# Optimization experiments

Measured on AMD Instinct MI355X. Metric: run time of the kernel, lower is better.

Reference implementation:

```python
import jax, jax.numpy as jnp
import numpy as np

N, E, DIN, GB, GD, LB, LD, G = 50000, 640000, 64, 128, 4, 256, 2, 1024


def setup_inputs() -> dict:
    key = jax.random.key(0)
    ks = jax.random.split(key, 20)
    p = lambda k, shape: (jax.random.normal(k, shape, dtype=jnp.float32) * 0.05)
    return {
        "x": jax.random.normal(ks[0], (N, DIN), dtype=jnp.float32),
        "edge_index": jax.random.randint(ks[1], (2, E), 0, N, dtype=jnp.int64),
        "batch": jnp.sort(jax.random.randint(ks[2], (N,), 0, G, dtype=jnp.int64)),
        "num_graphs": G,
        "W0": p(ks[3], (DIN, GB)), "b0": p(ks[4], (GB,)),
        "Wg": p(ks[5], (GD, GB, GB)), "bg": p(ks[6], (GD, GB)),
        "gamma_g": jnp.ones((GD, GB), jnp.float32), "beta_g": jnp.zeros((GD, GB), jnp.float32),
        "Wl0": p(ks[7], (GB, LB)), "bl0": p(ks[8], (LB,)),
        "Wl": p(ks[9], (LD, LB, LB)), "bl": p(ks[10], (LD, LB)),
        "gamma_l": jnp.ones((LD, LB), jnp.float32), "beta_l": jnp.zeros((LD, LB), jnp.float32),
        "Wout": p(ks[11], (LB, 2)), "bout": p(ks[12], (2,)),
    }


def reference(x, edge_index, batch, num_graphs, W0, b0, Wg, bg, gamma_g, beta_g,
              Wl0, bl0, Wl, bl, gamma_l, beta_l, Wout, bout):
    n = x.shape[0]
    src, dst = edge_index[0], edge_index[1]
    # GCN degree normalization with self loops: deg = 1 + in-degree
    deg = jax.ops.segment_sum(jnp.ones(src.shape[0], x.dtype), dst, num_segments=n) + 1.0
    dinv = jax.lax.rsqrt(deg)                 # deg^{-1/2}
    enorm = dinv[src] * dinv[dst]             # [E] edge norm
    snorm = dinv * dinv                       # [N] self-loop norm (deg^{-1})

    def gcn(h, W, b):
        hw = h @ W                                            # [N, GB]
        agg = jax.ops.segment_sum(hw[src] * enorm[:, None], dst, num_segments=n)
        return agg + hw * snorm[:, None] + b

    def bn(h, g, bt):  # training-mode batchnorm (biased var), eps=1e-5
        m = h.mean(0)
        v = h.var(0)
        return (h - m) * jax.lax.rsqrt(v + 1e-5) * g + bt

    h = jax.nn.relu(gcn(x, W0, b0))
    for i in range(Wg.shape[0]):
        h = jax.nn.relu(bn(gcn(h, Wg[i], bg[i]), gamma_g[i], beta_g[i]))
    # global_add_pool
    hp = jax.ops.segment_sum(h, batch, num_segments=num_graphs)  # [G, GB]
    h = jax.nn.relu(hp @ Wl0 + bl0)
    for i in range(Wl.shape[0]):
        h = jax.nn.relu(bn(h @ Wl[i] + bl[i], gamma_l[i], beta_l[i]))
    return h @ Wout + bout
```

## Files before the change

kernel.cpp:

```cpp
#include <hip/hip_runtime.h>

#define NN 50000
#define EE 640000
#define DINv 64
#define GBv 128
#define GDv 4
#define LBv 256
#define LDv 2
#define GGv 1024

#define NB 196
#define BCAP 4096
#define BTILE 4096
#define NBT ((EE + BTILE - 1) / BTILE)

#define NTILES ((NN + 63) / 64)
#define UPN (NN * 16)
#define CONVN (DINv * GBv + GDv * GBv * GBv)

typedef _Float16 f16x8 __attribute__((ext_vector_type(8)));
typedef float f32x4 __attribute__((ext_vector_type(4)));

__device__ __forceinline__ float h2f(ushort u) {
  union { ushort u; _Float16 h; } x;
  x.u = u;
  return (float)x.h;
}
__device__ __forceinline__ ushort f2h(float f) {
  union { ushort u; _Float16 h; } x;
  x.h = (_Float16)f;
  return x.u;
}


__global__ __launch_bounds__(256) void k_bucket(const int* __restrict__ ei,
                                                int* __restrict__ bcnt,
                                                uint* __restrict__ bkt) {
  __shared__ int lcnt[NB];
  __shared__ int lbase[NB];
  __shared__ int gbase[NB];
  __shared__ int ls[256];
  __shared__ uint stage[BTILE];
  __shared__ ushort sb[BTILE];
  int tid = threadIdx.x;
  int t0 = blockIdx.x * BTILE;
  int cnt = min(BTILE, EE - t0);
  for (int i = tid; i < NB; i += 256) lcnt[i] = 0;
  __syncthreads();

  uint en[16];
  int bb[16], rk[16];
  int nper = (cnt + 255) >> 8;
  for (int k = 0; k < nper; k++) {
    int e = k * 256 + tid;
    if (e < cnt) {
      int src = ei[t0 + e];
      int dst = ei[EE + t0 + e];
      int b = dst >> 8;
      en[k] = ((uint)src << 8) | (uint)(dst & 255);
      bb[k] = b;
      rk[k] = atomicAdd(&lcnt[b], 1);
    } else {
      bb[k] = -1;
    }
  }
  __syncthreads();

  int v = (tid < NB) ? lcnt[tid] : 0;
  ls[tid] = v;
  __syncthreads();
  for (int off = 1; off < 256; off <<= 1) {
    int t = (tid >= off) ? ls[tid - off] : 0;
    __syncthreads();
    ls[tid] += t;
    __syncthreads();
  }
  if (tid < NB) {
    lbase[tid] = ls[tid] - v;
    gbase[tid] = atomicAdd(&bcnt[tid], v);
  }
  __syncthreads();

  for (int k = 0; k < nper; k++) {
    if (bb[k] >= 0) {
      int slot = lbase[bb[k]] + rk[k];
      stage[slot] = en[k];
      sb[slot] = (ushort)bb[k];
    }
  }
  __syncthreads();

  for (int i = tid; i < cnt; i += 256) {
    int b = sb[i];
    bkt[(size_t)b * BCAP + gbase[b] + (i - lbase[b])] = stage[i];
  }
}


__global__ __launch_bounds__(256) void k_csr(const uint* __restrict__ bkt,
                                             const int* __restrict__ bcnt,
                                             int* __restrict__ offs,
                                             float* __restrict__ dinv,
                                             int* __restrict__ col,
                                             int* __restrict__ deg,
                                             int* __restrict__ ghist) {
  __shared__ int lhist[256];
  __shared__ int lofs[256];
  __shared__ int lcur[256];
  __shared__ int lsb[256];
  __shared__ int lh2[64];
  int b = blockIdx.x;
  int tid = threadIdx.x;
  int bv = (tid < NB) ? bcnt[tid] : 0;
  lsb[tid] = bv;
  lhist[tid] = 0;
  if (tid < 64) lh2[tid] = 0;
  __syncthreads();
  for (int off = 1; off < 256; off <<= 1) {
    int t = (tid >= off) ? lsb[tid - off] : 0;
    __syncthreads();
    lsb[tid] += t;
    __syncthreads();
  }
  int cnt = bcnt[b];
  int base = lsb[b] - cnt;
  const uint* B = bkt + (size_t)b * BCAP;
  for (int i = tid; i < cnt; i += 256) atomicAdd(&lhist[B[i] & 255], 1);
  __syncthreads();
  int v = lhist[tid];
  lofs[tid] = v;
  __syncthreads();
  for (int off = 1; off < 256; off <<= 1) {
    int t = (tid >= off) ? lofs[tid - off] : 0;
    __syncthreads();
    lofs[tid] += t;
    __syncthreads();
  }
  int excl = lofs[tid] - v;
  int n = b * 256 + tid;
  if (n < NN) {
    offs[n] = base + excl;
    dinv[n] = rsqrtf((float)(v + 1));
    int d = min(v, 63);
    deg[n] = d;
    atomicAdd(&lh2[d], 1);
  }
  lcur[tid] = excl;
  __syncthreads();
  if (tid < 64 && lh2[tid]) atomicAdd(&ghist[tid], lh2[tid]);
  if (b == 0 && tid == 0) offs[NN] = EE;
  for (int i = tid; i < cnt; i += 256) {
    uint e = B[i];
    int p = atomicAdd(&lcur[e & 255], 1);
    col[base + p] = (int)(e >> 8);
  }
}


__global__ __launch_bounds__(256) void k_dperm(const int* __restrict__ deg,
                                               const int* __restrict__ ghist,
                                               int* __restrict__ gcur,
                                               int* __restrict__ perm) {
  __shared__ int lhist[64];
  __shared__ int lbase[64];
  int tid = threadIdx.x;
  if (tid < 64) lhist[tid] = 0;
  __syncthreads();
  int n = blockIdx.x * 256 + tid;
  int d = 0, rk = 0;
  if (n < NN) {
    d = deg[n];
    rk = atomicAdd(&lhist[d], 1);
  }
  __syncthreads();
  if (tid < 64) {
    int s = 0;
    for (int i = tid + 1; i < 64; i++) s += ghist[i];
    if (lhist[tid]) lbase[tid] = s + atomicAdd(&gcur[tid], lhist[tid]);
  }
  __syncthreads();
  if (n < NN) perm[lbase[d] + rk] = n;
}


__global__ __launch_bounds__(256) void k_prep(const float* __restrict__ x,
                                              const float* __restrict__ dinv,
                                              const float* __restrict__ W0,
                                              const float* __restrict__ Wg,
                                              ushort* __restrict__ u,
                                              ushort* __restrict__ Wt0,
                                              ushort* __restrict__ Wtg) {
  int idx = blockIdx.x * 256 + threadIdx.x;
  if (idx < UPN) {
    int n = idx >> 4;
    float4 v = ((const float4*)x)[idx];
    float d = dinv[n];
    union { ushort us[4]; uint2 q; } o;
    o.us[0] = f2h(v.x * d);
    o.us[1] = f2h(v.y * d);
    o.us[2] = f2h(v.z * d);
    o.us[3] = f2h(v.w * d);
    ((uint2*)u)[idx] = o.q;
  } else {
    int j = idx - UPN;
    if (j < DINv * GBv) {
      int c = j >> 6, k = j & 63;
      Wt0[j] = f2h(W0[k * GBv + c]);
    } else if (j < CONVN) {
      int e = j - DINv * GBv;
      int i = e >> 14, rem = e & 16383;
      int c = rem >> 7, k = rem & 127;
      Wtg[e] = f2h(Wg[i * GBv * GBv + k * GBv + c]);
    }
  }
}


template <int K, int MODE, bool STATS, bool OUTF>
__global__ __launch_bounds__(512, 4) void k_layer(const ushort* __restrict__ Gin,
                                                  const int* __restrict__ col,
                                                  const int* __restrict__ offs,
                                                  const float* __restrict__ dinv,
                                                  const int* __restrict__ perm,
                                                  const float* __restrict__ st,
                                                  const float* __restrict__ gamma,
                                                  const float* __restrict__ beta,
                                                  const ushort* __restrict__ Wt,
                                                  const float* __restrict__ bias,
                                                  float* __restrict__ stG,
                                                  ushort* __restrict__ Gout) {
  constexpr int VEC = K / 16;
  constexpr int KP = K + 8;
  constexpr int CP = 136;
  constexpr bool REUSE = (K == 128);
  __shared__ __attribute__((aligned(16))) _Float16 sW[128 * KP];
  __shared__ __attribute__((aligned(16))) _Float16 sA[64 * KP];
  __shared__ float sB[128], sS[128], sT[128];
  __shared__ float ssum[128], ssq[128];
  __shared__ float sDn[64];
  _Float16* sC = REUSE ? sA : sW;
  int tid = threadIdx.x;

  {
    constexpr int CH = K / 8;
    for (int i = tid; i < 128 * CH; i += 512) {
      int c = i / CH, ch = i - c * CH;
      *(uint4*)&sW[c * KP + ch * 8] = ((const uint4*)Wt)[i];
    }
  }
  if (tid < 128) {
    sB[tid] = bias[tid];
    if constexpr (STATS) {
      ssum[tid] = 0.f;
      ssq[tid] = 0.f;
    }
    if constexpr (MODE == 2) {
      float mu = st[tid] * (1.f / NN);
      float var = st[128 + tid] * (1.f / NN) - mu * mu;
      float s = rsqrtf(var + 1e-5f) * gamma[tid];
      sS[tid] = s;
      sT[tid] = beta[tid] - mu * s;
    }
  }
  if constexpr (MODE == 2) __syncthreads();

  int w = tid >> 6, lane = tid & 63;
  int quad = lane >> 4, m = lane & 15;
  int row0 = blockIdx.x * 64;

  float sc[VEC], tc[VEC];
  if constexpr (MODE == 2) {
#pragma unroll
    for (int v = 0; v < VEC; v++) {
      sc[v] = sS[m * VEC + v];
      tc[v] = sT[m * VEC + v];
    }
  }

  union U { uint4 v4; uint2 v2; ushort us[8]; };
  auto loadrow = [&](int s) {
    U u;
    const ushort* p = Gin + (long)s * K + m * VEC;
    if constexpr (VEC == 8) u.v4 = *(const uint4*)p;
    else u.v2 = *(const uint2*)p;
    return u;
  };

  for (int rnd = 0; rnd < 2; rnd++) {
    int r = rnd * 32 + w * 4 + quad;
    int idx = row0 + r;
    float acc[VEC];
#pragma unroll
    for (int v = 0; v < VEC; v++) acc[v] = 0.f;
    float dn = 0.f;
    if (idx < NN) {
      int n = perm[idx];
      dn = dinv[n];
      auto addrow = [&](U u, float wv) {
#pragma unroll
        for (int v = 0; v < VEC; v++) {
          float g = h2f(u.us[v]);
          if constexpr (MODE == 2) g = fmaxf(g * sc[v] + tc[v], 0.f);
          else if constexpr (MODE == 1) g = fmaxf(g, 0.f);
          acc[v] += g * wv;
        }
      };
      addrow(loadrow(n), (MODE == 0) ? 1.f : dn);
      int s0 = offs[n], s1 = offs[n + 1];
      for (int j = s0; j < s1; j += 8) {
        int si[8];
#pragma unroll
        for (int t = 0; t < 8; t++) {
          int jj = j + t;
          si[t] = col[jj < s1 ? jj : s1 - 1];
        }
        U uu[8];
#pragma unroll
        for (int t = 0; t < 8; t++) uu[t] = loadrow(si[t]);
        float wt[8];
#pragma unroll
        for (int t = 0; t < 8; t++) {
          float base = (MODE == 0) ? 1.f : dinv[si[t]];
          wt[t] = (j + t < s1) ? base : 0.f;
        }
#pragma unroll
        for (int t = 0; t < 8; t++) addrow(uu[t], wt[t]);
      }
    }
    if constexpr (OUTF) {
      if (m == 0) sDn[r] = dn;
    }
    U o;
#pragma unroll
    for (int v = 0; v < VEC; v++) o.us[v] = f2h(acc[v] * dn);
    _Float16* ap = &sA[r * KP + m * VEC];
    if constexpr (VEC == 8) *(uint4*)ap = o.v4;
    else *(uint2*)ap = o.v2;
  }
  __syncthreads();

  int wr = w >> 1, wc = w & 1;
  f32x4 acc2[4];
#pragma unroll
  for (int ct = 0; ct < 4; ct++) acc2[ct] = (f32x4){0.f, 0.f, 0.f, 0.f};
  const _Float16* pa = &sA[(16 * wr + m) * KP + quad * 8];
#pragma unroll
  for (int ks = 0; ks < K; ks += 32) {
    f16x8 a = *(const f16x8*)(pa + ks);
#pragma unroll
    for (int ct = 0; ct < 4; ct++) {
      int c = wc * 64 + ct * 16 + m;
      f16x8 bfr = *(const f16x8*)&sW[c * KP + ks + quad * 8];
      acc2[ct] = __builtin_amdgcn_mfma_f32_16x16x32_f16(a, bfr, acc2[ct], 0, 0, 0);
    }
  }

  int crow = 16 * wr + quad * 4;
  float ps[4], pq[4];
  if constexpr (STATS) {
#pragma unroll
    for (int ct = 0; ct < 4; ct++) {
      int c = wc * 64 + ct * 16 + m;
      float bb = sB[c];
      ps[ct] = 0.f;
      pq[ct] = 0.f;
#pragma unroll
      for (int r = 0; r < 4; r++) {
        if (row0 + crow + r < NN) {
          float g = acc2[ct][r] + bb;
          ps[ct] += g;
          pq[ct] += g * g;
        }
      }
    }
  }
  __syncthreads();

  float dvr[4];
  if constexpr (OUTF) {
#pragma unroll
    for (int r = 0; r < 4; r++) dvr[r] = sDn[crow + r];
  }
#pragma unroll
  for (int ct = 0; ct < 4; ct++) {
    int c = wc * 64 + ct * 16 + m;
    float bb = sB[c];
#pragma unroll
    for (int r = 0; r < 4; r++) {
      float y = acc2[ct][r] + bb;
      if constexpr (OUTF) y = fmaxf(y, 0.f) * dvr[r];
      sC[(crow + r) * CP + c] = (_Float16)y;
    }
  }
  __syncthreads();

  {
    int r = tid >> 3;
    int c0 = (tid & 7) * 16;
    int idx2 = row0 + r;
    if (idx2 < NN) {
      int node = perm[idx2];
      const uint4* srcp = (const uint4*)&sC[r * CP + c0];
      uint4* dst = (uint4*)(Gout + (long)node * 128 + c0);
      dst[0] = srcp[0];
      dst[1] = srcp[1];
    }
  }

  if constexpr (STATS) {
#pragma unroll
    for (int ct = 0; ct < 4; ct++) {
      float s = ps[ct], q = pq[ct];
      s += __shfl_xor(s, 16);
      q += __shfl_xor(q, 16);
      s += __shfl_xor(s, 32);
      q += __shfl_xor(q, 32);
      if (quad == 0) {
        atomicAdd(&ssum[wc * 64 + ct * 16 + m], s);
        atomicAdd(&ssq[wc * 64 + ct * 16 + m], q);
      }
    }
    __syncthreads();
    if (tid < 128) {
      int c = (tid + blockIdx.x * 8) & 127;
      atomicAdd(&stG[c], ssum[c]);
      atomicAdd(&stG[128 + c], ssq[c]);
    }
  }
}


__global__ __launch_bounds__(128) void k_pool2(const ushort* __restrict__ G,
                                               const float* __restrict__ st,
                                               const float* __restrict__ gamma,
                                               const float* __restrict__ beta,
                                               const int* __restrict__ batch,
                                               float* __restrict__ hp) {
  __shared__ int sse[2];
  int g = blockIdx.x;
  int c = threadIdx.x;
  if (c < 2) {
    int key = g + c;
    int lo = 0, hi = NN;
    while (lo < hi) {
      int mid = (lo + hi) >> 1;
      if (batch[mid] < key) lo = mid + 1;
      else hi = mid;
    }
    sse[c] = lo;
  }
  __syncthreads();
  int s = sse[0], e = sse[1];
  float m = st[c] * (1.f / NN);
  float v = st[128 + c] * (1.f / NN) - m * m;
  float sc = rsqrtf(v + 1e-5f) * gamma[c];
  float tc = beta[c] - m * sc;
  float a0 = 0.f, a1 = 0.f, a2 = 0.f, a3 = 0.f;
  int n = s;
  for (; n + 3 < e; n += 4) {
    float g0 = h2f(G[(long)(n + 0) * 128 + c]);
    float g1 = h2f(G[(long)(n + 1) * 128 + c]);
    float g2 = h2f(G[(long)(n + 2) * 128 + c]);
    float g3 = h2f(G[(long)(n + 3) * 128 + c]);
    a0 += fmaxf(g0 * sc + tc, 0.f);
    a1 += fmaxf(g1 * sc + tc, 0.f);
    a2 += fmaxf(g2 * sc + tc, 0.f);
    a3 += fmaxf(g3 * sc + tc, 0.f);
  }
  for (; n < e; n++) a0 += fmaxf(h2f(G[(long)n * 128 + c]) * sc + tc, 0.f);
  hp[(long)g * 128 + c] = (a0 + a1) + (a2 + a3);
}


__global__ void k_colstats(const float* __restrict__ X, int rows, float* __restrict__ st) {
  int c = threadIdx.x;
  int C = blockDim.x;
  float s = 0.f, q = 0.f;
  for (int r = blockIdx.x; r < rows; r += gridDim.x) {
    float v = X[(long)r * C + c];
    s += v;
    q += v * v;
  }
  atomicAdd(&st[c], s);
  atomicAdd(&st[C + c], q);
}


template <int KIN, int MODE>
__global__ __launch_bounds__(256) void k_fc(const float* __restrict__ X,
                                            const float* __restrict__ W,
                                            const float* __restrict__ b,
                                            const float* __restrict__ st,
                                            const float* __restrict__ gamma,
                                            const float* __restrict__ beta,
                                            float* __restrict__ Y) {
  __shared__ float sx[KIN];
  int g = blockIdx.x;
  int c = threadIdx.x;
  for (int k = c; k < KIN; k += 256) {
    float v = X[(long)g * KIN + k];
    if constexpr (MODE == 2) {
      float m = st[k] * (1.f / GGv);
      float var = st[KIN + k] * (1.f / GGv) - m * m;
      v = fmaxf((v - m) * rsqrtf(var + 1e-5f) * gamma[k] + beta[k], 0.f);
    }
    sx[k] = v;
  }
  __syncthreads();
  float acc = b[c];
#pragma unroll 8
  for (int k = 0; k < KIN; k++) acc += sx[k] * W[(long)k * 256 + c];
  Y[(long)g * 256 + c] = (MODE == 0) ? fmaxf(acc, 0.f) : acc;
}

__global__ __launch_bounds__(256) void k_out(const float* __restrict__ X,
                                             const float* __restrict__ st,
                                             const float* __restrict__ gamma,
                                             const float* __restrict__ beta,
                                             const float* __restrict__ Wout,
                                             const float* __restrict__ bout,
                                             float* __restrict__ out) {
  int g = blockIdx.x * 4 + (threadIdx.x >> 6);
  int l = threadIdx.x & 63;
  float a0 = 0.f, a1 = 0.f;
  for (int k = l; k < LBv; k += 64) {
    float z = X[(long)g * LBv + k];
    float m = st[k] * (1.f / GGv);
    float var = st[LBv + k] * (1.f / GGv) - m * m;
    float x = fmaxf((z - m) * rsqrtf(var + 1e-5f) * gamma[k] + beta[k], 0.f);
    a0 += x * Wout[2 * k];
    a1 += x * Wout[2 * k + 1];
  }
  for (int off = 32; off > 0; off >>= 1) {
    a0 += __shfl_down(a0, off);
    a1 += __shfl_down(a1, off);
  }
  if (l == 0) {
    out[2 * g] = a0 + bout[0];
    out[2 * g + 1] = a1 + bout[1];
  }
}


extern "C" void kernel_launch(void* const* d_in, const int* in_sizes, int n_in,
                              void* d_out, int out_size, void* d_ws, size_t ws_size,
                              hipStream_t stream) {
  const float* x = (const float*)d_in[0];
  const int* ei = (const int*)d_in[1];
  const int* batch = (const int*)d_in[2];
  const float* W0 = (const float*)d_in[4];
  const float* b0 = (const float*)d_in[5];
  const float* Wg = (const float*)d_in[6];
  const float* bg = (const float*)d_in[7];
  const float* gamma_g = (const float*)d_in[8];
  const float* beta_g = (const float*)d_in[9];
  const float* Wl0 = (const float*)d_in[10];
  const float* bl0 = (const float*)d_in[11];
  const float* Wl = (const float*)d_in[12];
  const float* bl = (const float*)d_in[13];
  const float* gamma_l = (const float*)d_in[14];
  const float* beta_l = (const float*)d_in[15];
  const float* Wout = (const float*)d_in[16];
  const float* bout = (const float*)d_in[17];
  float* out = (float*)d_out;

  char* w = (char*)d_ws;
  auto alloc = [&](size_t bytes) {
    void* p = (void*)w;
    w += (bytes + 255) & ~(size_t)255;
    return p;
  };
  int* bcnt = (int*)alloc((size_t)NB * 4);
  float* stAll = (float*)alloc((size_t)(4 * 256 + 2 * 512) * 4);
  int* ghist = (int*)alloc((size_t)64 * 4);
  int* gcur = (int*)alloc((size_t)64 * 4);
  size_t zspan = (char*)w - (char*)bcnt;
  uint* bkt = (uint*)alloc((size_t)NB * BCAP * 4);
  int* offs = (int*)alloc((size_t)(NN + 1) * 4);
  int* col = (int*)alloc((size_t)EE * 4);
  float* dinv = (float*)alloc((size_t)NN * 4);
  int* deg = (int*)alloc((size_t)NN * 4);
  int* perm = (int*)alloc((size_t)NN * 4);
  ushort* u = (ushort*)alloc((size_t)NN * DINv * 2);
  ushort* g1 = (ushort*)alloc((size_t)NN * GBv * 2);
  ushort* g2 = (ushort*)alloc((size_t)NN * GBv * 2);
  ushort* Wt0 = (ushort*)alloc((size_t)DINv * GBv * 2);
  ushort* Wtg = (ushort*)alloc((size_t)GDv * GBv * GBv * 2);
  float* hp = (float*)alloc((size_t)GGv * GBv * 4);
  float* m1 = (float*)alloc((size_t)GGv * LBv * 4);
  float* m2 = (float*)alloc((size_t)GGv * LBv * 4);

  float* stg = stAll;
  float* sth0 = stAll + 4 * 256;
  float* sth1 = sth0 + 512;

  hipMemsetAsync(bcnt, 0, zspan, stream);

  k_bucket<<<NBT, 256, 0, stream>>>(ei, bcnt, bkt);
  k_csr<<<NB, 256, 0, stream>>>(bkt, bcnt, offs, dinv, col, deg, ghist);
  k_dperm<<<NB, 256, 0, stream>>>(deg, ghist, gcur, perm);
  k_prep<<<(UPN + CONVN + 255) / 256, 256, 0, stream>>>(x, dinv, W0, Wg, u, Wt0, Wtg);

  k_layer<64, 0, false, true><<<NTILES, 512, 0, stream>>>(
      u, col, offs, dinv, perm, nullptr, nullptr, nullptr, Wt0, b0, nullptr, g1);
  k_layer<128, 0, true, false><<<NTILES, 512, 0, stream>>>(
      g1, col, offs, dinv, perm, nullptr, nullptr, nullptr, Wtg, bg, stg, g2);
  for (int i = 1; i < GDv; i++) {
    const ushort* gin = (i & 1) ? g2 : g1;
    ushort* gout = (i & 1) ? g1 : g2;
    k_layer<128, 2, true, false><<<NTILES, 512, 0, stream>>>(
        gin, col, offs, dinv, perm, stg + (size_t)(i - 1) * 256,
        gamma_g + (size_t)(i - 1) * GBv, beta_g + (size_t)(i - 1) * GBv,
        Wtg + (size_t)i * GBv * GBv, bg + (size_t)i * GBv, stg + (size_t)i * 256, gout);
  }

  k_pool2<<<GGv, 128, 0, stream>>>(g1, stg + 3 * 256, gamma_g + 3 * GBv, beta_g + 3 * GBv,
                                   batch, hp);

  k_fc<GBv, 0><<<GGv, 256, 0, stream>>>(hp, Wl0, bl0, nullptr, nullptr, nullptr, m1);
  k_fc<LBv, 1><<<GGv, 256, 0, stream>>>(m1, Wl, bl, nullptr, nullptr, nullptr, m2);
  k_colstats<<<256, LBv, 0, stream>>>(m2, GGv, sth0);
  k_fc<LBv, 2><<<GGv, 256, 0, stream>>>(m2, Wl + (size_t)LBv * LBv, bl + LBv, sth0,
                                        gamma_l, beta_l, m1);
  k_colstats<<<256, LBv, 0, stream>>>(m1, GGv, sth1);
  k_out<<<GGv / 4, 256, 0, stream>>>(m1, sth1, gamma_l + LBv, beta_l + LBv, Wout, bout, out);
}
```

Measured before the change: 417.2 us.

## Pad CSR rows to multiples of eight with a zero dummy node

Each node's adjacency list in the CSR is padded to a multiple of 8. The padding points to a dummy node NN whose feature rows are zeroed and whose dinv is 0. The gather loop can then read column indices as aligned int4 pairs and drop the per-edge bounds checks and clamping. Separately, the BN scale and shift are now computed in registers per thread instead of through shared memory plus a barrier, and launch bounds rise from 4 to 6 blocks per SM. The cost is extra buffer space, padding writes in k_csr, and register pressure from the higher occupancy target.

After: 493.9 us. +18.4%, slower.

```diff
diff --git a/kernel.cpp b/kernel.cpp
--- a/kernel.cpp
+++ b/kernel.cpp
@@ -17,6 +17,7 @@
 #define NTILES ((NN + 63) / 64)
 #define UPN (NN * 16)
 #define CONVN (DINv * GBv + GDv * GBv * GBv)
+#define ZEXT 320
 
 typedef _Float16 f16x8 __attribute__((ext_vector_type(8)));
 typedef float f32x4 __attribute__((ext_vector_type(4)));
@@ -123,12 +124,14 @@
     __syncthreads();
   }
   int cnt = bcnt[b];
-  int base = lsb[b] - cnt;
+  int rawbase = lsb[b] - cnt;
+  int pbase = ((rawbase + 7) & ~7) + b * 2048;
   const uint* B = bkt + (size_t)b * BCAP;
   for (int i = tid; i < cnt; i += 256) atomicAdd(&lhist[B[i] & 255], 1);
   __syncthreads();
   int v = lhist[tid];
-  lofs[tid] = v;
+  int pv = (v + 7) & ~7;
+  lofs[tid] = pv;
   __syncthreads();
   for (int off = 1; off < 256; off <<= 1) {
     int t = (tid >= off) ? lofs[tid - off] : 0;
@@ -136,23 +139,23 @@
     lofs[tid] += t;
     __syncthreads();
   }
-  int excl = lofs[tid] - v;
+  int excl = lofs[tid] - pv;
   int n = b * 256 + tid;
   if (n < NN) {
-    offs[n] = base + excl;
+    offs[n] = pbase + excl;
     dinv[n] = rsqrtf((float)(v + 1));
-    int d = min(v, 63);
-    deg[n] = d;
-    atomicAdd(&lh2[d], 1);
+    deg[n] = v;
+    atomicAdd(&lh2[min(v, 63)], 1);
+    for (int k = v; k < pv; k++) col[pbase + excl + k] = NN;
   }
   lcur[tid] = excl;
   __syncthreads();
   if (tid < 64 && lh2[tid]) atomicAdd(&ghist[tid], lh2[tid]);
-  if (b == 0 && tid == 0) offs[NN] = EE;
+  if (b == 0 && tid == 0) dinv[NN] = 0.f;
   for (int i = tid; i < cnt; i += 256) {
     uint e = B[i];
     int p = atomicAdd(&lcur[e & 255], 1);
-    col[base + p] = (int)(e >> 8);
+    col[pbase + p] = (int)(e >> 8);
   }
 }
 
@@ -169,7 +172,7 @@
   int n = blockIdx.x * 256 + tid;
   int d = 0, rk = 0;
   if (n < NN) {
-    d = deg[n];
+    d = min(deg[n], 63);
     rk = atomicAdd(&lhist[d], 1);
   }
   __syncthreads();
@@ -189,7 +192,9 @@
                                               const float* __restrict__ Wg,
                                               ushort* __restrict__ u,
                                               ushort* __restrict__ Wt0,
-                                              ushort* __restrict__ Wtg) {
+                                              ushort* __restrict__ Wtg,
+                                              ushort* __restrict__ g1,
+                                              ushort* __restrict__ g2) {
   int idx = blockIdx.x * 256 + threadIdx.x;
   if (idx < UPN) {
     int n = idx >> 4;
@@ -211,15 +216,21 @@
       int i = e >> 14, rem = e & 16383;
       int c = rem >> 7, k = rem & 127;
       Wtg[e] = f2h(Wg[i * GBv * GBv + k * GBv + c]);
+    } else if (j < CONVN + ZEXT) {
+      int z = j - CONVN;
+      if (z < 64) u[(size_t)NN * DINv + z] = 0;
+      else if (z < 192) g1[(size_t)NN * GBv + (z - 64)] = 0;
+      else g2[(size_t)NN * GBv + (z - 192)] = 0;
     }
   }
 }
 
 
 template <int K, int MODE, bool STATS, bool OUTF>
-__global__ __launch_bounds__(512, 4) void k_layer(const ushort* __restrict__ Gin,
+__global__ __launch_bounds__(512, 6) void k_layer(const ushort* __restrict__ Gin,
                                                   const int* __restrict__ col,
                                                   const int* __restrict__ offs,
+                                                  const int* __restrict__ deg,
                                                   const float* __restrict__ dinv,
                                                   const int* __restrict__ perm,
                                                   const float* __restrict__ st,
@@ -235,7 +246,7 @@
   constexpr bool REUSE = (K == 128);
   __shared__ __attribute__((aligned(16))) _Float16 sW[128 * KP];
   __shared__ __attribute__((aligned(16))) _Float16 sA[64 * KP];
-  __shared__ float sB[128], sS[128], sT[128];
+  __shared__ float sB[128];
   __shared__ float ssum[128], ssq[128];
   __shared__ float sDn[64];
   _Float16* sC = REUSE ? sA : sW;
@@ -254,15 +265,7 @@
       ssum[tid] = 0.f;
       ssq[tid] = 0.f;
     }
-    if constexpr (MODE == 2) {
-      float mu = st[tid] * (1.f / NN);
-      float var = st[128 + tid] * (1.f / NN) - mu * mu;
-      float s = rsqrtf(var + 1e-5f) * gamma[tid];
-      sS[tid] = s;
-      sT[tid] = beta[tid] - mu * s;
-    }
-  }
-  if constexpr (MODE == 2) __syncthreads();
+  }
 
   int w = tid >> 6, lane = tid & 63;
   int quad = lane >> 4, m = lane & 15;
@@ -272,8 +275,12 @@
   if constexpr (MODE == 2) {
 #pragma unroll
     for (int v = 0; v < VEC; v++) {
-      sc[v] = sS[m * VEC + v];
-      tc[v] = sT[m * VEC + v];
+      int c = m * VEC + v;
+      float mu = st[c] * (1.f / NN);
+      float var = st[128 + c] * (1.f / NN) - mu * mu;
+      float s = rsqrtf(var + 1e-5f) * gamma[c];
+      sc[v] = s;
+      tc[v] = beta[c] - mu * s;
     }
   }
 
@@ -306,23 +313,19 @@
         }
       };
       addrow(loadrow(n), (MODE == 0) ? 1.f : dn);
-      int s0 = offs[n], s1 = offs[n + 1];
-      for (int j = s0; j < s1; j += 8) {
-        int si[8];
-#pragma unroll
-        for (int t = 0; t < 8; t++) {
-          int jj = j + t;
-          si[t] = col[jj < s1 ? jj : s1 - 1];
-        }
+      int s0 = offs[n];
+      int pcnt = (deg[n] + 7) & ~7;
+      const int* cp = col + s0;
+      for (int j = 0; j < pcnt; j += 8) {
+        int4 ca = *(const int4*)(cp + j);
+        int4 cb = *(const int4*)(cp + j + 4);
+        int si[8] = {ca.x, ca.y, ca.z, ca.w, cb.x, cb.y, cb.z, cb.w};
         U uu[8];
 #pragma unroll
         for (int t = 0; t < 8; t++) uu[t] = loadrow(si[t]);
         float wt[8];
 #pragma unroll
-        for (int t = 0; t < 8; t++) {
-          float base = (MODE == 0) ? 1.f : dinv[si[t]];
-          wt[t] = (j + t < s1) ? base : 0.f;
-        }
+        for (int t = 0; t < 8; t++) wt[t] = (MODE == 0) ? 1.f : dinv[si[t]];
 #pragma unroll
         for (int t = 0; t < 8; t++) addrow(uu[t], wt[t]);
       }
@@ -577,13 +580,13 @@
   size_t zspan = (char*)w - (char*)bcnt;
   uint* bkt = (uint*)alloc((size_t)NB * BCAP * 4);
   int* offs = (int*)alloc((size_t)(NN + 1) * 4);
-  int* col = (int*)alloc((size_t)EE * 4);
-  float* dinv = (float*)alloc((size_t)NN * 4);
+  int* col = (int*)alloc((size_t)(EE + NB * 2048 + 8192) * 4);
+  float* dinv = (float*)alloc((size_t)(NN + 1) * 4);
   int* deg = (int*)alloc((size_t)NN * 4);
   int* perm = (int*)alloc((size_t)NN * 4);
-  ushort* u = (ushort*)alloc((size_t)NN * DINv * 2);
-  ushort* g1 = (ushort*)alloc((size_t)NN * GBv * 2);
-  ushort* g2 = (ushort*)alloc((size_t)NN * GBv * 2);
+  ushort* u = (ushort*)alloc((size_t)(NN + 1) * DINv * 2);
+  ushort* g1 = (ushort*)alloc((size_t)(NN + 1) * GBv * 2);
+  ushort* g2 = (ushort*)alloc((size_t)(NN + 1) * GBv * 2);
   ushort* Wt0 = (ushort*)alloc((size_t)DINv * GBv * 2);
   ushort* Wtg = (ushort*)alloc((size_t)GDv * GBv * GBv * 2);
   float* hp = (float*)alloc((size_t)GGv * GBv * 4);
@@ -599,17 +602,18 @@
   k_bucket<<<NBT, 256, 0, stream>>>(ei, bcnt, bkt);
   k_csr<<<NB, 256, 0, stream>>>(bkt, bcnt, offs, dinv, col, deg, ghist);
   k_dperm<<<NB, 256, 0, stream>>>(deg, ghist, gcur, perm);
-  k_prep<<<(UPN + CONVN + 255) / 256, 256, 0, stream>>>(x, dinv, W0, Wg, u, Wt0, Wtg);
+  k_prep<<<(UPN + CONVN + ZEXT + 255) / 256, 256, 0, stream>>>(x, dinv, W0, Wg, u, Wt0,
+                                                               Wtg, g1, g2);
 
   k_layer<64, 0, false, true><<<NTILES, 512, 0, stream>>>(
-      u, col, offs, dinv, perm, nullptr, nullptr, nullptr, Wt0, b0, nullptr, g1);
+      u, col, offs, deg, dinv, perm, nullptr, nullptr, nullptr, Wt0, b0, nullptr, g1);
   k_layer<128, 0, true, false><<<NTILES, 512, 0, stream>>>(
-      g1, col, offs, dinv, perm, nullptr, nullptr, nullptr, Wtg, bg, stg, g2);
+      g1, col, offs, deg, dinv, perm, nullptr, nullptr, nullptr, Wtg, bg, stg, g2);
   for (int i = 1; i < GDv; i++) {
     const ushort* gin = (i & 1) ? g2 : g1;
     ushort* gout = (i & 1) ? g1 : g2;
     k_layer<128, 2, true, false><<<NTILES, 512, 0, stream>>>(
-        gin, col, offs, dinv, perm, stg + (size_t)(i - 1) * 256,
+        gin, col, offs, deg, dinv, perm, stg + (size_t)(i - 1) * 256,
         gamma_g + (size_t)(i - 1) * GBv, beta_g + (size_t)(i - 1) * GBv,
         Wtg + (size_t)i * GBv * GBv, bg + (size_t)i * GBv, stg + (size_t)i * 256, gout);
   }
```
